# Optimization experiments

Hardware: AMD Instinct MI355X
Metric: run time of the kernel (lower is better)

The kernel has to match this reference:

```python
import jax, jax.numpy as jnp
import numpy as np


def setup_inputs() -> dict:
    key = jax.random.key(0)
    k1, k2, k3 = jax.random.split(key, 3)
    B, F, D = 1024, 784, 512
    x = jax.random.normal(k1, (B, F), dtype=jnp.float32)
    # keras 'uniform' initializer ~ U(-0.05, 0.05)
    Wmin = jax.random.uniform(k2, (D, F), dtype=jnp.float32, minval=-0.05, maxval=0.05)
    Wmax = jax.random.uniform(k3, (D, F), dtype=jnp.float32, minval=-0.05, maxval=0.05)
    return {"x": x, "Wmin": Wmin, "Wmax": Wmax}


def reference(x, Wmin, Wmax):
    # x: [B, F]; Wmin, Wmax: [D, F]
    # L1[b,d] = min_f (x[b,f] - Wmin[d,f]); L2[b,d] = min_f (Wmax[d,f] - x[b,f])
    L1 = jnp.min(x[:, None, :] - Wmin[None, :, :], axis=2)  # [B, D]
    L2 = jnp.min(Wmax[None, :, :] - x[:, None, :], axis=2)  # [B, D]
    # activation is None (linear) in this config
    return jnp.minimum(L1, L2)  # [B, D]
```

## Files before the change

### kernel.cpp

```cpp
#include <hip/hip_runtime.h>


constexpr int F_DIM = 784;
constexpr int BM = 64;
constexpr int BN = 64;
constexpr int BK = 16;
constexpr int LSTR = BK + 4;
constexpr int NCHUNK = F_DIM / BK;
constexpr int ZSPLIT = 7;
constexpr int CPZ = NCHUNK / ZSPLIT;

typedef float f4v __attribute__((ext_vector_type(4)));
typedef float f2v __attribute__((ext_vector_type(2)));

__global__ __launch_bounds__(256, 4)
void dendral_init_kernel(float* __restrict__ out) {
  const int i = blockIdx.x * 256 + threadIdx.x;
  const float inf = __builtin_inff();
  f4v v = {inf, inf, inf, inf};
  ((f4v*)out)[i] = v;
}

__device__ inline void atomic_min_float(float* addr, float v) {
  if (v >= 0.0f) atomicMin((int*)addr, __float_as_int(v));
  else           atomicMax((unsigned int*)addr, __float_as_uint(v));
}

__global__ __launch_bounds__(256, 2)
void dendral_min_kernel(const float* __restrict__ x,
                        const float* __restrict__ wmin,
                        const float* __restrict__ wmax,
                        float* __restrict__ out, int D) {
  __shared__ float lx[2][BM * LSTR];
  __shared__ float lwn[2][BN * LSTR];
  __shared__ float lwx[2][BN * LSTR];

  const int t  = threadIdx.x;
  const int tx = t & 15;
  const int ty = t >> 4;
  const int b0 = blockIdx.x * BM;
  const int d0 = blockIdx.y * BN;
  const int c0 = blockIdx.z * CPZ;
  const int c1 = c0 + CPZ;

  const int xr = t >> 2;
  const int xc = (t & 3) << 2;
  const int wt = t >> 7;
  const int wr = (t & 127) >> 1;
  const int wc = (t & 1) << 3;

  const float* xg = x + (size_t)(b0 + xr) * F_DIM + xc;
  const float* wg = (wt ? wmax : wmin) + (size_t)(d0 + wr) * F_DIM + wc;
  float* lds_x = &lx[0][xr * LSTR + xc];
  float* lds_w = (wt ? &lwx[0][0] : &lwn[0][0]) + wr * LSTR + wc;
  constexpr int BUFSTRIDE_X = BM * LSTR;
  constexpr int BUFSTRIDE_W = BN * LSTR;

  f4v px  = *(const f4v*)(xg + c0 * BK);
  f4v pw0 = *(const f4v*)(wg + c0 * BK);
  f4v pw1 = *(const f4v*)(wg + c0 * BK + 4);
  *(f4v*)(lds_x) = px;
  *(f4v*)(lds_w) = pw0;
  *(f4v*)(lds_w + 4) = pw1;
  __syncthreads();

  float acc[4][4];
#pragma unroll
  for (int r = 0; r < 4; ++r)
#pragma unroll
    for (int c = 0; c < 4; ++c)
      acc[r][c] = __builtin_inff();

  int cur = 0;
  for (int kc = c0; kc < c1; ++kc) {
    const bool more = (kc + 1 < c1);
    if (more) {
      px  = *(const f4v*)(xg + (kc + 1) * BK);
      pw0 = *(const f4v*)(wg + (kc + 1) * BK);
      pw1 = *(const f4v*)(wg + (kc + 1) * BK + 4);
    }

    const float* lxb = &lx[cur][ty * LSTR];
    const float* lnb = &lwn[cur][tx * LSTR];
    const float* lwb = &lwx[cur][tx * LSTR];
#pragma unroll
    for (int f = 0; f < BK; f += 4) {
      f4v nv[4], wv[4];
#pragma unroll
      for (int c = 0; c < 4; ++c) {
        nv[c] = *(const f4v*)&lnb[c * 16 * LSTR + f];
        wv[c] = *(const f4v*)&lwb[c * 16 * LSTR + f];
      }
#pragma unroll
      for (int r = 0; r < 4; ++r) {
        const f4v xv = *(const f4v*)&lxb[r * 16 * LSTR + f];
#pragma unroll
        for (int c = 0; c < 4; ++c) {
          f2v d1lo = xv.xy - nv[c].xy;
          f2v d1hi = xv.zw - nv[c].zw;
          f2v d2lo = wv[c].xy - xv.xy;
          f2v d2hi = wv[c].zw - xv.zw;
          float t1 = fminf(fminf(d1lo.x, d1lo.y), d1hi.x);
          float t2 = fminf(fminf(d1hi.y, d2lo.x), d2lo.y);
          float t3 = fminf(fminf(d2hi.x, d2hi.y), acc[r][c]);
          acc[r][c] = fminf(fminf(t1, t2), t3);
        }
      }
    }

    if (more) {
      const int nxt = cur ^ 1;
      *(f4v*)(lds_x + nxt * BUFSTRIDE_X) = px;
      *(f4v*)(lds_w + nxt * BUFSTRIDE_W) = pw0;
      *(f4v*)(lds_w + nxt * BUFSTRIDE_W + 4) = pw1;
      cur = nxt;
    }
    __syncthreads();
  }

#pragma unroll
  for (int r = 0; r < 4; ++r)
#pragma unroll
    for (int c = 0; c < 4; ++c) {
      const int b = b0 + ty + 16 * r;
      const int d = d0 + tx + 16 * c;
      atomic_min_float(&out[(size_t)b * D + d], acc[r][c]);
    }
}

extern "C" void kernel_launch(void* const* d_in, const int* in_sizes, int n_in,
                              void* d_out, int out_size, void* d_ws, size_t ws_size,
                              hipStream_t stream) {
  const float* x    = (const float*)d_in[0];
  const float* wmin = (const float*)d_in[1];
  const float* wmax = (const float*)d_in[2];
  float* out = (float*)d_out;
  const int B = in_sizes[0] / F_DIM;
  const int D = in_sizes[1] / F_DIM;

  dendral_init_kernel<<<(B * D) / 1024, 256, 0, stream>>>(out);

  dim3 grid(B / BM, D / BN, ZSPLIT);
  dendral_min_kernel<<<grid, 256, 0, stream>>>(x, wmin, wmax, out, D);
  (void)n_in; (void)d_ws; (void)ws_size; (void)out_size;
}
```

Baseline: 96.57 us.

## Load x directly from global memory and halve K chunk, doubling z-split

Removes the LDS staging of x: each thread now reads its four x rows straight from global memory (cached) inside the compute loop, so only the weight tiles go through shared memory. BK drops from 16 to 8 and ZSPLIT rises from 7 to 14, which keeps the chunks per block at 7 and doubles the grid size. The intent is to cut LDS traffic and footprint and to raise parallelism. In exchange, global/L1 loads now sit in the inner loop without prefetching, and the extra z-split doubles the atomic-min traffic on the output.

```diff
diff --git a/kernel.cpp b/kernel.cpp
--- a/kernel.cpp
+++ b/kernel.cpp
@@ -4,10 +4,10 @@
 constexpr int F_DIM = 784;
 constexpr int BM = 64;
 constexpr int BN = 64;
-constexpr int BK = 16;
+constexpr int BK = 8;
 constexpr int LSTR = BK + 4;
 constexpr int NCHUNK = F_DIM / BK;
-constexpr int ZSPLIT = 7;
+constexpr int ZSPLIT = 14;
 constexpr int CPZ = NCHUNK / ZSPLIT;
 
 typedef float f4v __attribute__((ext_vector_type(4)));
@@ -31,7 +31,6 @@
                         const float* __restrict__ wmin,
                         const float* __restrict__ wmax,
                         float* __restrict__ out, int D) {
-  __shared__ float lx[2][BM * LSTR];
   __shared__ float lwn[2][BN * LSTR];
   __shared__ float lwx[2][BN * LSTR];
 
@@ -43,25 +42,21 @@
   const int c0 = blockIdx.z * CPZ;
   const int c1 = c0 + CPZ;
 
-  const int xr = t >> 2;
-  const int xc = (t & 3) << 2;
   const int wt = t >> 7;
   const int wr = (t & 127) >> 1;
-  const int wc = (t & 1) << 3;
+  const int wc = (t & 1) << 2;
 
-  const float* xg = x + (size_t)(b0 + xr) * F_DIM + xc;
   const float* wg = (wt ? wmax : wmin) + (size_t)(d0 + wr) * F_DIM + wc;
-  float* lds_x = &lx[0][xr * LSTR + xc];
   float* lds_w = (wt ? &lwx[0][0] : &lwn[0][0]) + wr * LSTR + wc;
-  constexpr int BUFSTRIDE_X = BM * LSTR;
   constexpr int BUFSTRIDE_W = BN * LSTR;
 
-  f4v px  = *(const f4v*)(xg + c0 * BK);
-  f4v pw0 = *(const f4v*)(wg + c0 * BK);
-  f4v pw1 = *(const f4v*)(wg + c0 * BK + 4);
-  *(f4v*)(lds_x) = px;
-  *(f4v*)(lds_w) = pw0;
-  *(f4v*)(lds_w + 4) = pw1;
+  const float* xp0 = x + (size_t)(b0 + ty)      * F_DIM;
+  const float* xp1 = x + (size_t)(b0 + ty + 16) * F_DIM;
+  const float* xp2 = x + (size_t)(b0 + ty + 32) * F_DIM;
+  const float* xp3 = x + (size_t)(b0 + ty + 48) * F_DIM;
+
+  f4v pw = *(const f4v*)(wg + c0 * BK);
+  *(f4v*)lds_w = pw;
   __syncthreads();
 
   float acc[4][4];
@@ -74,17 +69,18 @@
   int cur = 0;
   for (int kc = c0; kc < c1; ++kc) {
     const bool more = (kc + 1 < c1);
-    if (more) {
-      px  = *(const f4v*)(xg + (kc + 1) * BK);
-      pw0 = *(const f4v*)(wg + (kc + 1) * BK);
-      pw1 = *(const f4v*)(wg + (kc + 1) * BK + 4);
-    }
+    if (more)
+      pw = *(const f4v*)(wg + (kc + 1) * BK);
 
-    const float* lxb = &lx[cur][ty * LSTR];
     const float* lnb = &lwn[cur][tx * LSTR];
     const float* lwb = &lwx[cur][tx * LSTR];
 #pragma unroll
     for (int f = 0; f < BK; f += 4) {
+      f4v xv[4];
+      xv[0] = *(const f4v*)(xp0 + kc * BK + f);
+      xv[1] = *(const f4v*)(xp1 + kc * BK + f);
+      xv[2] = *(const f4v*)(xp2 + kc * BK + f);
+      xv[3] = *(const f4v*)(xp3 + kc * BK + f);
       f4v nv[4], wv[4];
 #pragma unroll
       for (int c = 0; c < 4; ++c) {
@@ -92,27 +88,23 @@
         wv[c] = *(const f4v*)&lwb[c * 16 * LSTR + f];
       }
 #pragma unroll
-      for (int r = 0; r < 4; ++r) {
-        const f4v xv = *(const f4v*)&lxb[r * 16 * LSTR + f];
+      for (int r = 0; r < 4; ++r)
 #pragma unroll
         for (int c = 0; c < 4; ++c) {
-          f2v d1lo = xv.xy - nv[c].xy;
-          f2v d1hi = xv.zw - nv[c].zw;
-          f2v d2lo = wv[c].xy - xv.xy;
-          f2v d2hi = wv[c].zw - xv.zw;
+          f2v d1lo = xv[r].xy - nv[c].xy;
+          f2v d1hi = xv[r].zw - nv[c].zw;
+          f2v d2lo = wv[c].xy - xv[r].xy;
+          f2v d2hi = wv[c].zw - xv[r].zw;
           float t1 = fminf(fminf(d1lo.x, d1lo.y), d1hi.x);
           float t2 = fminf(fminf(d1hi.y, d2lo.x), d2lo.y);
           float t3 = fminf(fminf(d2hi.x, d2hi.y), acc[r][c]);
           acc[r][c] = fminf(fminf(t1, t2), t3);
         }
-      }
     }
 
     if (more) {
       const int nxt = cur ^ 1;
-      *(f4v*)(lds_x + nxt * BUFSTRIDE_X) = px;
-      *(f4v*)(lds_w + nxt * BUFSTRIDE_W) = pw0;
-      *(f4v*)(lds_w + nxt * BUFSTRIDE_W + 4) = pw1;
+      *(f4v*)(lds_w + nxt * BUFSTRIDE_W) = pw;
       cur = nxt;
     }
     __syncthreads();
```

New measurement: 99.44 us. 3.0% more time.
